# Optimization experiments

Hardware: AMD Instinct MI355X
Metric: run time of the kernel (lower is better)

Reference implementation:

```python
import jax, jax.numpy as jnp
import numpy as np

N_NODES = 100000
N_EDGES = 1600000
NUM_FEATURES = 256
HIDDEN_DIM = 128
NUM_CLASSES = 16


def setup_inputs() -> dict:
    key = jax.random.key(0)
    k1, k2, k3, k4 = jax.random.split(key, 4)
    x = jax.random.normal(k1, (N_NODES, NUM_FEATURES), dtype=jnp.float32)
    edge_index = jax.random.randint(k2, (2, N_EDGES), 0, N_NODES, dtype=jnp.int64)
    # Glorot-style init like PyG GCNConv's Linear
    W1 = jax.random.normal(k3, (NUM_FEATURES, HIDDEN_DIM), dtype=jnp.float32) / np.sqrt(NUM_FEATURES)
    b1 = jnp.zeros((HIDDEN_DIM,), dtype=jnp.float32)
    W2 = jax.random.normal(k4, (HIDDEN_DIM, NUM_CLASSES), dtype=jnp.float32) / np.sqrt(HIDDEN_DIM)
    b2 = jnp.zeros((NUM_CLASSES,), dtype=jnp.float32)
    return {"x": x, "edge_index": edge_index, "W1": W1, "b1": b1, "W2": W2, "b2": b2}


def _gcn_norm(edge_index, num_nodes):
    """PyG GCNConv default: add self-loops, symmetric deg^{-1/2} A deg^{-1/2} norm."""
    loops = jnp.arange(num_nodes, dtype=edge_index.dtype)
    row = jnp.concatenate([edge_index[0], loops])  # source
    col = jnp.concatenate([edge_index[1], loops])  # target
    deg = jax.ops.segment_sum(jnp.ones_like(col, dtype=jnp.float32), col,
                              num_segments=num_nodes)
    dinv = jnp.where(deg > 0, jax.lax.rsqrt(deg), 0.0)
    norm = dinv[row] * dinv[col]  # [E + N]
    return row, col, norm


def _gcn_conv(h, row, col, norm, num_nodes):
    # transform first (PyG: lin then propagate), then normalized sum-aggregate
    msg = h[row] * norm[:, None]            # [E+N, d] gather + scale
    return jax.ops.segment_sum(msg, col, num_segments=num_nodes)


def reference(x, edge_index, W1, b1, W2, b2):
    num_nodes = x.shape[0]
    row, col, norm = _gcn_norm(edge_index, num_nodes)
    h = x @ W1
    h = _gcn_conv(h, row, col, norm, num_nodes) + b1
    h = jax.nn.relu(h)
    h = h @ W2
    out = _gcn_conv(h, row, col, norm, num_nodes) + b2
    return out
```

## Files before the change

### kernel.cpp

```cpp
#include <hip/hip_runtime.h>

#define N_NODES 100000
#define N_EDGES 1600000
#define F_IN    256
#define F_HID   128
#define F_OUT   16

#define BSHIFT  9
#define BNODES  512
#define NB      196
#define ECAP    16384
#define CHUNK   4096
#define NCHUNK  ((N_EDGES + CHUNK - 1) / CHUNK)

typedef __attribute__((ext_vector_type(8))) short short8;
typedef __attribute__((ext_vector_type(4))) float float4v;

__device__ __forceinline__ unsigned int bf16_rn(float f) {
    unsigned int u = __float_as_uint(f);
    return (u + 0x7FFFu + ((u >> 16) & 1u)) >> 16;
}
__device__ __forceinline__ unsigned int cvtpk(float lo, float hi) {
    unsigned int r;
    asm("v_cvt_pk_bf16_f32 %0, %1, %2" : "=v"(r) : "v"(lo), "v"(hi));
    return r;
}
__device__ __forceinline__ float blo(unsigned int u) { return __uint_as_float(u << 16); }
__device__ __forceinline__ float bhi(unsigned int u) { return __uint_as_float(u & 0xFFFF0000u); }
__device__ __forceinline__ float bfu(unsigned short u) { return __uint_as_float(((unsigned int)u) << 16); }


__global__ __launch_bounds__(256) void k_binit(int* __restrict__ bcur) {
    int i = threadIdx.x;
    if (i < NB) bcur[i] = i * ECAP;
}

__global__ __launch_bounds__(256) void k_binscatter(const int* __restrict__ rowi,
                                                    const int* __restrict__ coli,
                                                    int* __restrict__ bcur,
                                                    unsigned int* __restrict__ ebuf) {
    __shared__ int cnt[NB], gbase[NB], run[NB];
    int tid = threadIdx.x;
    int e0 = blockIdx.x * CHUNK;
    for (int i = tid; i < NB; i += 256) { cnt[i] = 0; run[i] = 0; }
    __syncthreads();
    int d[16], s[16];
    #pragma unroll
    for (int i = 0; i < 16; i++) {
        int e = e0 + i * 256 + tid;
        if (e < N_EDGES) {
            d[i] = coli[e]; s[i] = rowi[e];
            atomicAdd(&cnt[d[i] >> BSHIFT], 1);
        } else d[i] = -1;
    }
    __syncthreads();
    for (int i = tid; i < NB; i += 256)
        gbase[i] = cnt[i] ? atomicAdd(&bcur[i], cnt[i]) : 0;
    __syncthreads();
    #pragma unroll
    for (int i = 0; i < 16; i++) {
        if (d[i] >= 0) {
            int b = d[i] >> BSHIFT;
            int off = atomicAdd(&run[b], 1);
            ebuf[gbase[b] + off] = ((unsigned int)(d[i] & 511) << 17) | (unsigned int)s[i];
        }
    }
}

__global__ __launch_bounds__(512) void k_finalize(const int* __restrict__ bcur,
                                                  const unsigned int* __restrict__ ebuf,
                                                  int* __restrict__ rp_start,
                                                  int* __restrict__ rp_end,
                                                  float* __restrict__ dinv,
                                                  int* __restrict__ esrc) {
    __shared__ int ndeg[BNODES];
    __shared__ int sc[BNODES];
    int tid = threadIdx.x;
    int b   = blockIdx.x;
    int nb0 = b << BSHIFT;
    int ebeg = b * ECAP, eend = bcur[b];
    ndeg[tid] = 0;
    __syncthreads();
    for (int e = ebeg + tid; e < eend; e += 512)
        atomicAdd(&ndeg[ebuf[e] >> 17], 1);
    __syncthreads();
    sc[tid] = ndeg[tid];
    __syncthreads();
    for (int off = 1; off < BNODES; off <<= 1) {
        int v = (tid >= off) ? sc[tid - off] : 0;
        __syncthreads();
        sc[tid] += v;
        __syncthreads();
    }
    {
        int n = nb0 + tid;
        int deg = ndeg[tid];
        int excl = sc[tid] - deg;
        if (n < N_NODES) {
            rp_start[n] = ebeg + excl;
            rp_end[n]   = ebeg + excl + deg;
            dinv[n]     = rsqrtf(1.0f + (float)deg);
        }
        ndeg[tid] = excl;
    }
    __syncthreads();
    for (int e = ebeg + tid; e < eend; e += 512) {
        unsigned int p = ebuf[e];
        int off = atomicAdd(&ndeg[p >> 17], 1);
        esrc[ebeg + off] = (int)(p & 0x1FFFFu);
    }
}


__global__ __launch_bounds__(256) void k_transW(const float* __restrict__ W1,
                                                ushort* __restrict__ Wt) {
    int t = blockIdx.x * 256 + threadIdx.x;
    int c = t & 127, k = t >> 7;
    Wt[c * 256 + k] = (ushort)cvtpk(W1[k * 128 + c], 0.f);
}


__global__ __launch_bounds__(512) void k_gemm1(const float* __restrict__ x,
                                               const ushort* __restrict__ Wt,
                                               const float* __restrict__ dinv,
                                               ushort* __restrict__ g1) {
    __shared__ ushort Bl[128 * 256];
    const int tid = threadIdx.x;
    const int w = tid >> 6;
    const int l = tid & 63;
    const int m = l & 15;
    const int q = l >> 4;
    const int R0 = blockIdx.x * 256;

    {
        const uint4* Wg = (const uint4*)Wt;
        uint4* Bl4 = (uint4*)Bl;
        #pragma unroll
        for (int it = 0; it < 8; it++) {
            int i = it * 512 + tid;
            int c = i >> 5, j = i & 31;
            Bl4[c * 32 + (j ^ (c & 7))] = Wg[i];
        }
    }
    __syncthreads();

    int r0 = R0 + w * 32 + m;      if (r0 > N_NODES - 1) r0 = N_NODES - 1;
    int r1 = R0 + w * 32 + 16 + m; if (r1 > N_NODES - 1) r1 = N_NODES - 1;
    const float* xr0 = &x[(size_t)r0 * F_IN + q * 8];
    const float* xr1 = &x[(size_t)r1 * F_IN + q * 8];
    const short8* Bl8 = (const short8*)Bl;

    float4v acc[2][8];
    #pragma unroll
    for (int i = 0; i < 2; i++)
        #pragma unroll
        for (int j = 0; j < 8; j++) acc[i][j] = (float4v){0.f, 0.f, 0.f, 0.f};

    #pragma unroll 2
    for (int kt = 0; kt < F_IN; kt += 32) {
        float4 a0 = *(const float4*)&xr0[kt];
        float4 a1 = *(const float4*)&xr0[kt + 4];
        float4 b0 = *(const float4*)&xr1[kt];
        float4 b1 = *(const float4*)&xr1[kt + 4];
        short8 af0, af1;
        ((uint*)&af0)[0] = cvtpk(a0.x, a0.y); ((uint*)&af0)[1] = cvtpk(a0.z, a0.w);
        ((uint*)&af0)[2] = cvtpk(a1.x, a1.y); ((uint*)&af0)[3] = cvtpk(a1.z, a1.w);
        ((uint*)&af1)[0] = cvtpk(b0.x, b0.y); ((uint*)&af1)[1] = cvtpk(b0.z, b0.w);
        ((uint*)&af1)[2] = cvtpk(b1.x, b1.y); ((uint*)&af1)[3] = cvtpk(b1.z, b1.w);
        int jq = (kt >> 3) + q;
        #pragma unroll
        for (int n = 0; n < 8; n++) {
            int col = n * 16 + m;
            short8 bfr = Bl8[col * 32 + (jq ^ (col & 7))];
            acc[0][n] = __builtin_amdgcn_mfma_f32_16x16x32_bf16(af0, bfr, acc[0][n], 0, 0, 0);
            acc[1][n] = __builtin_amdgcn_mfma_f32_16x16x32_bf16(af1, bfr, acc[1][n], 0, 0, 0);
        }
    }

    const int rbase = R0 + w * 32 + q * 4;
    float dv0[4], dv1[4];
    #pragma unroll
    for (int r = 0; r < 4; r++) {
        int v0 = rbase + r;      dv0[r] = (v0 < N_NODES) ? dinv[v0] : 0.f;
        int v1 = rbase + 16 + r; dv1[r] = (v1 < N_NODES) ? dinv[v1] : 0.f;
    }
    #pragma unroll
    for (int n = 0; n < 8; n++) {
        #pragma unroll
        for (int r = 0; r < 4; r++) {
            int v0 = rbase + r;
            if (v0 < N_NODES) {
                float f = dv0[r] * acc[0][n][r];
                g1[v0 * F_HID + n * 16 + m] = (ushort)cvtpk(f, f);
            }
            int v1 = rbase + 16 + r;
            if (v1 < N_NODES) {
                float f = dv1[r] * acc[1][n][r];
                g1[v1 * F_HID + n * 16 + m] = (ushort)cvtpk(f, f);
            }
        }
    }
}


__global__ __launch_bounds__(256) void k_agg1g2(const int* __restrict__ rp_start,
                                                const int* __restrict__ rp_end,
                                                const int* __restrict__ esrc,
                                                const float* __restrict__ dinv,
                                                const unsigned int* __restrict__ g1,
                                                const float* __restrict__ b1,
                                                const float* __restrict__ W2,
                                                ushort* __restrict__ g2b,
                                                int nbase) {
    __shared__ float hl[4][132];
    const int tid  = threadIdx.x;
    const int wave = tid >> 6;
    const int lane = tid & 63;
    const int col  = lane & 15, part = lane >> 4;

    float w2r[32];
    #pragma unroll
    for (int i = 0; i < 32; i++) w2r[i] = W2[i * 64 + lane];

    float2 bb = ((const float2*)b1)[lane];

    #pragma unroll 1
    for (int j = 0; j < 4; j++) {
        const int node = nbase + blockIdx.x * 16 + j * 4 + wave;
        int s = rp_start[node], t = rp_end[node];
        unsigned int u = g1[node * 64 + lane];
        float ax = blo(u), ay = bhi(u);
        int e = s;
        for (; e + 7 < t; e += 8) {
            int r0 = esrc[e],     r1 = esrc[e + 1], r2 = esrc[e + 2], r3 = esrc[e + 3];
            int r4 = esrc[e + 4], r5 = esrc[e + 5], r6 = esrc[e + 6], r7 = esrc[e + 7];
            unsigned int u0 = g1[r0 * 64 + lane], u1 = g1[r1 * 64 + lane];
            unsigned int u2 = g1[r2 * 64 + lane], u3 = g1[r3 * 64 + lane];
            unsigned int u4 = g1[r4 * 64 + lane], u5 = g1[r5 * 64 + lane];
            unsigned int u6 = g1[r6 * 64 + lane], u7 = g1[r7 * 64 + lane];
            ax += blo(u0) + blo(u1) + blo(u2) + blo(u3)
                + blo(u4) + blo(u5) + blo(u6) + blo(u7);
            ay += bhi(u0) + bhi(u1) + bhi(u2) + bhi(u3)
                + bhi(u4) + bhi(u5) + bhi(u6) + bhi(u7);
        }
        for (; e + 3 < t; e += 4) {
            int r0 = esrc[e], r1 = esrc[e + 1], r2 = esrc[e + 2], r3 = esrc[e + 3];
            unsigned int u0 = g1[r0 * 64 + lane], u1 = g1[r1 * 64 + lane];
            unsigned int u2 = g1[r2 * 64 + lane], u3 = g1[r3 * 64 + lane];
            ax += blo(u0) + blo(u1) + blo(u2) + blo(u3);
            ay += bhi(u0) + bhi(u1) + bhi(u2) + bhi(u3);
        }
        for (; e < t; e++) {
            unsigned int u0 = g1[esrc[e] * 64 + lane];
            ax += blo(u0); ay += bhi(u0);
        }
        float wv = dinv[node];
        hl[wave][lane * 2]     = fmaxf(fmaf(wv, ax, bb.x), 0.0f);
        hl[wave][lane * 2 + 1] = fmaxf(fmaf(wv, ay, bb.y), 0.0f);

        float acc = 0.f;
        #pragma unroll
        for (int i = 0; i < 32; i++)
            acc = fmaf(hl[wave][i * 4 + part], w2r[i], acc);
        acc += __shfl_xor(acc, 16);
        acc += __shfl_xor(acc, 32);
        if (lane < 16) g2b[node * 16 + col] = (ushort)bf16_rn(wv * acc);
    }
}


__global__ __launch_bounds__(256) void k_agg2(const int* __restrict__ rp_start,
                                              const int* __restrict__ rp_end,
                                              const int* __restrict__ esrc,
                                              const float* __restrict__ dinv,
                                              const ushort* __restrict__ g2b,
                                              const float* __restrict__ b2,
                                              float* __restrict__ out) {
    int gid = blockIdx.x * 256 + threadIdx.x;
    int node = gid >> 4;
    int f = gid & 15;
    if (node >= N_NODES) return;
    int s = rp_start[node], t = rp_end[node];
    float acc = bfu(g2b[node * 16 + f]);
    int e = s;
    for (; e + 7 < t; e += 8) {
        float a0 = bfu(g2b[esrc[e] * 16 + f]),     a1 = bfu(g2b[esrc[e + 1] * 16 + f]);
        float a2 = bfu(g2b[esrc[e + 2] * 16 + f]), a3 = bfu(g2b[esrc[e + 3] * 16 + f]);
        float a4 = bfu(g2b[esrc[e + 4] * 16 + f]), a5 = bfu(g2b[esrc[e + 5] * 16 + f]);
        float a6 = bfu(g2b[esrc[e + 6] * 16 + f]), a7 = bfu(g2b[esrc[e + 7] * 16 + f]);
        acc += a0 + a1 + a2 + a3 + a4 + a5 + a6 + a7;
    }
    for (; e + 3 < t; e += 4) {
        acc += bfu(g2b[esrc[e] * 16 + f]) + bfu(g2b[esrc[e + 1] * 16 + f])
             + bfu(g2b[esrc[e + 2] * 16 + f]) + bfu(g2b[esrc[e + 3] * 16 + f]);
    }
    for (; e < t; e++) acc += bfu(g2b[esrc[e] * 16 + f]);
    out[node * 16 + f] = fmaf(dinv[node], acc, b2[f]);
}


extern "C" void kernel_launch(void* const* d_in, const int* in_sizes, int n_in,
                              void* d_out, int out_size, void* d_ws, size_t ws_size,
                              hipStream_t stream) {
    const float* x   = (const float*)d_in[0];
    const int*   ei  = (const int*)d_in[1];
    const float* W1  = (const float*)d_in[2];
    const float* b1  = (const float*)d_in[3];
    const float* W2  = (const float*)d_in[4];
    const float* b2  = (const float*)d_in[5];
    float* out = (float*)d_out;

    const int* rowi = ei;
    const int* coli = ei + N_EDGES;

    char* ws = (char*)d_ws;
    int*          bcur     = (int*)(ws + 0);
    int*          rp_start = (int*)(ws + 8192);
    int*          rp_end   = (int*)(ws + 524288);
    float*        dinv     = (float*)(ws + 1048576);
    unsigned int* ebuf     = (unsigned int*)(ws + 2097152);
    int*          esrc     = (int*)(ws + 16777216);
    ushort*       Wt       = (ushort*)(ws + 31457280);
    ushort*       g1       = (ushort*)(ws + 33554432);
    ushort*       g2b      = (ushort*)(ws + 62914560);

    k_binit     <<<1, 256, 0, stream>>>(bcur);
    k_binscatter<<<NCHUNK, 256, 0, stream>>>(rowi, coli, bcur, ebuf);
    k_finalize  <<<NB, 512, 0, stream>>>(bcur, ebuf, rp_start, rp_end, dinv, esrc);
    k_transW    <<<128, 256, 0, stream>>>(W1, Wt);

    k_gemm1     <<<(N_NODES + 255) / 256, 512, 0, stream>>>(x, Wt, dinv, g1);
    k_agg1g2    <<<N_NODES / 32, 256, 0, stream>>>(rp_start, rp_end, esrc, dinv,
                                                   (const unsigned int*)g1, b1, W2, g2b, 0);
    k_agg1g2    <<<N_NODES / 32, 256, 0, stream>>>(rp_start, rp_end, esrc, dinv,
                                                   (const unsigned int*)g1, b1, W2, g2b,
                                                   N_NODES / 2);
    k_agg2      <<<(N_NODES * 16 + 255) / 256, 256, 0, stream>>>(rp_start, rp_end, esrc,
                                                                 dinv, g2b, b2, out);
}
```

Measured before the change: 320.5 us.

## Stage binscatter writes in LDS, vectorize agg2 to bf16 pairs, split agg1 into quarters

The edge binning kernel now runs an LDS prefix scan over bucket counts and stages each chunk's packed edges in shared memory sorted by bucket. It then writes them to the global bucket buffer in contiguous runs instead of scattered single stores. The second aggregation has each thread handle two features through 32-bit loads, which halves the gather instructions and thread count. The first aggregation is launched as four quarter-range launches with a bounds check, replacing two halves. This trades extra LDS use and barriers for better write coalescing and fewer loads.

```diff
diff --git a/kernel.cpp b/kernel.cpp
--- a/kernel.cpp
+++ b/kernel.cpp
@@ -39,9 +39,14 @@
                                                     const int* __restrict__ coli,
                                                     int* __restrict__ bcur,
                                                     unsigned int* __restrict__ ebuf) {
-    __shared__ int cnt[NB], gbase[NB], run[NB];
+    __shared__ int cnt[NB], gbase[NB], sbase[NB], run[NB];
+    __shared__ int sc[256];
+    __shared__ unsigned int wrd[CHUNK];
+    __shared__ unsigned char bkt[CHUNK];
     int tid = threadIdx.x;
     int e0 = blockIdx.x * CHUNK;
+    int tot = (e0 + CHUNK <= N_EDGES) ? CHUNK : (N_EDGES - e0);
+
     for (int i = tid; i < NB; i += 256) { cnt[i] = 0; run[i] = 0; }
     __syncthreads();
     int d[16], s[16];
@@ -54,6 +59,15 @@
         } else d[i] = -1;
     }
     __syncthreads();
+    sc[tid] = (tid < NB) ? cnt[tid] : 0;
+    __syncthreads();
+    for (int off = 1; off < 256; off <<= 1) {
+        int v = (tid >= off) ? sc[tid - off] : 0;
+        __syncthreads();
+        sc[tid] += v;
+        __syncthreads();
+    }
+    if (tid < NB) sbase[tid] = sc[tid] - cnt[tid];
     for (int i = tid; i < NB; i += 256)
         gbase[i] = cnt[i] ? atomicAdd(&bcur[i], cnt[i]) : 0;
     __syncthreads();
@@ -62,8 +76,15 @@
         if (d[i] >= 0) {
             int b = d[i] >> BSHIFT;
             int off = atomicAdd(&run[b], 1);
-            ebuf[gbase[b] + off] = ((unsigned int)(d[i] & 511) << 17) | (unsigned int)s[i];
-        }
+            int slot = sbase[b] + off;
+            wrd[slot] = ((unsigned int)(d[i] & 511) << 17) | (unsigned int)s[i];
+            bkt[slot] = (unsigned char)b;
+        }
+    }
+    __syncthreads();
+    for (int sl = tid; sl < tot; sl += 256) {
+        int b = bkt[sl];
+        ebuf[gbase[b] + (sl - sbase[b])] = wrd[sl];
     }
 }
 
@@ -211,7 +232,7 @@
                                                 const float* __restrict__ b1,
                                                 const float* __restrict__ W2,
                                                 ushort* __restrict__ g2b,
-                                                int nbase) {
+                                                int nbase, int nend) {
     __shared__ float hl[4][132];
     const int tid  = threadIdx.x;
     const int wave = tid >> 6;
@@ -227,6 +248,7 @@
     #pragma unroll 1
     for (int j = 0; j < 4; j++) {
         const int node = nbase + blockIdx.x * 16 + j * 4 + wave;
+        if (node >= nend) continue;
         int s = rp_start[node], t = rp_end[node];
         unsigned int u = g1[node * 64 + lane];
         float ax = blo(u), ay = bhi(u);
@@ -276,26 +298,44 @@
                                               const ushort* __restrict__ g2b,
                                               const float* __restrict__ b2,
                                               float* __restrict__ out) {
+    const unsigned int* g2u = (const unsigned int*)g2b;
     int gid = blockIdx.x * 256 + threadIdx.x;
-    int node = gid >> 4;
-    int f = gid & 15;
+    int node = gid >> 3;
+    int fp = gid & 7;
     if (node >= N_NODES) return;
     int s = rp_start[node], t = rp_end[node];
-    float acc = bfu(g2b[node * 16 + f]);
+    unsigned int u = g2u[node * 8 + fp];
+    float ax = blo(u), ay = bhi(u);
     int e = s;
     for (; e + 7 < t; e += 8) {
-        float a0 = bfu(g2b[esrc[e] * 16 + f]),     a1 = bfu(g2b[esrc[e + 1] * 16 + f]);
-        float a2 = bfu(g2b[esrc[e + 2] * 16 + f]), a3 = bfu(g2b[esrc[e + 3] * 16 + f]);
-        float a4 = bfu(g2b[esrc[e + 4] * 16 + f]), a5 = bfu(g2b[esrc[e + 5] * 16 + f]);
-        float a6 = bfu(g2b[esrc[e + 6] * 16 + f]), a7 = bfu(g2b[esrc[e + 7] * 16 + f]);
-        acc += a0 + a1 + a2 + a3 + a4 + a5 + a6 + a7;
+        int r0 = esrc[e],     r1 = esrc[e + 1], r2 = esrc[e + 2], r3 = esrc[e + 3];
+        int r4 = esrc[e + 4], r5 = esrc[e + 5], r6 = esrc[e + 6], r7 = esrc[e + 7];
+        unsigned int u0 = g2u[r0 * 8 + fp], u1 = g2u[r1 * 8 + fp];
+        unsigned int u2 = g2u[r2 * 8 + fp], u3 = g2u[r3 * 8 + fp];
+        unsigned int u4 = g2u[r4 * 8 + fp], u5 = g2u[r5 * 8 + fp];
+        unsigned int u6 = g2u[r6 * 8 + fp], u7 = g2u[r7 * 8 + fp];
+        ax += blo(u0) + blo(u1) + blo(u2) + blo(u3)
+            + blo(u4) + blo(u5) + blo(u6) + blo(u7);
+        ay += bhi(u0) + bhi(u1) + bhi(u2) + bhi(u3)
+            + bhi(u4) + bhi(u5) + bhi(u6) + bhi(u7);
     }
     for (; e + 3 < t; e += 4) {
-        acc += bfu(g2b[esrc[e] * 16 + f]) + bfu(g2b[esrc[e + 1] * 16 + f])
-             + bfu(g2b[esrc[e + 2] * 16 + f]) + bfu(g2b[esrc[e + 3] * 16 + f]);
-    }
-    for (; e < t; e++) acc += bfu(g2b[esrc[e] * 16 + f]);
-    out[node * 16 + f] = fmaf(dinv[node], acc, b2[f]);
+        int r0 = esrc[e], r1 = esrc[e + 1], r2 = esrc[e + 2], r3 = esrc[e + 3];
+        unsigned int u0 = g2u[r0 * 8 + fp], u1 = g2u[r1 * 8 + fp];
+        unsigned int u2 = g2u[r2 * 8 + fp], u3 = g2u[r3 * 8 + fp];
+        ax += blo(u0) + blo(u1) + blo(u2) + blo(u3);
+        ay += bhi(u0) + bhi(u1) + bhi(u2) + bhi(u3);
+    }
+    for (; e < t; e++) {
+        unsigned int u0 = g2u[esrc[e] * 8 + fp];
+        ax += blo(u0); ay += bhi(u0);
+    }
+    float wv = dinv[node];
+    float2 bb = ((const float2*)b2)[fp];
+    float2 o;
+    o.x = fmaf(wv, ax, bb.x);
+    o.y = fmaf(wv, ay, bb.y);
+    *(float2*)&out[node * 16 + fp * 2] = o;
 }
 
 
@@ -330,11 +370,12 @@
     k_transW    <<<128, 256, 0, stream>>>(W1, Wt);
 
     k_gemm1     <<<(N_NODES + 255) / 256, 512, 0, stream>>>(x, Wt, dinv, g1);
-    k_agg1g2    <<<N_NODES / 32, 256, 0, stream>>>(rp_start, rp_end, esrc, dinv,
-                                                   (const unsigned int*)g1, b1, W2, g2b, 0);
-    k_agg1g2    <<<N_NODES / 32, 256, 0, stream>>>(rp_start, rp_end, esrc, dinv,
-                                                   (const unsigned int*)g1, b1, W2, g2b,
-                                                   N_NODES / 2);
-    k_agg2      <<<(N_NODES * 16 + 255) / 256, 256, 0, stream>>>(rp_start, rp_end, esrc,
-                                                                 dinv, g2b, b2, out);
-}
+    for (int qd = 0; qd < 4; qd++) {
+        int nbase = qd * 25000;
+        k_agg1g2 <<<(25000 + 15) / 16, 256, 0, stream>>>(rp_start, rp_end, esrc, dinv,
+                                                         (const unsigned int*)g1, b1, W2,
+                                                         g2b, nbase, nbase + 25000);
+    }
+    k_agg2      <<<(N_NODES * 8 + 255) / 256, 256, 0, stream>>>(rp_start, rp_end, esrc,
+                                                                dinv, g2b, b2, out);
+}
```

After: 324.7 us. Within noise of the previous version (+1.3%).
